# Performance work log

Measured on AMD Instinct MI355X. Metric: run time of the kernel, lower is better.

The kernel has to match this reference:

```python
import jax, jax.numpy as jnp
import numpy as np

B, N, DIM, T, H, DH = 4, 2048, 512, 16, 8, 64
EPS = 1e-5


def setup_inputs() -> dict:
    key = jax.random.key(0)
    ks = jax.random.split(key, 7)
    x = jax.random.normal(ks[0], (B, N, DIM), dtype=jnp.float32)
    # time-distance matrix, e.g. months between scans, in [0, 24)
    R = jax.random.uniform(ks[1], (B, T, T), dtype=jnp.float32) * 24.0
    gamma = jnp.ones((DIM,), dtype=jnp.float32)
    beta = jnp.zeros((DIM,), dtype=jnp.float32)
    W_qkv = jax.random.normal(ks[2], (DIM, 3 * H * DH), dtype=jnp.float32) * 0.02
    W_out = jax.random.normal(ks[3], (H * DH, DIM), dtype=jnp.float32) * 0.02
    a = jax.random.uniform(ks[4], (H,), dtype=jnp.float32)          # torch.rand(heads)
    c = 12.0 * jax.random.uniform(ks[5], (H,), dtype=jnp.float32)   # 12 * torch.rand(heads)
    return {"x": x, "R": R, "gamma": gamma, "beta": beta,
            "W_qkv": W_qkv, "W_out": W_out, "a": a, "c": c}


def reference(x, R, gamma, beta, W_qkv, W_out, a, c):
    b, n, dim = x.shape
    t = R.shape[-1]
    num_patches = n // t
    scale = DH ** -0.5

    # LayerNorm
    mu = jnp.mean(x, axis=-1, keepdims=True)
    var = jnp.mean(jnp.square(x - mu), axis=-1, keepdims=True)
    xn = (x - mu) * jax.lax.rsqrt(var + EPS) * gamma + beta

    # QKV projection -> [b, h, n, d]
    qkv = xn @ W_qkv  # [b, n, 3*h*d]
    q, k, v = jnp.split(qkv, 3, axis=-1)
    def to_heads(z):
        return z.reshape(b, n, H, DH).transpose(0, 2, 1, 3)
    q, k, v = to_heads(q), to_heads(k), to_heads(v)

    # attention scores with ReLU then learned sigmoid time-decay mask
    dots = jnp.einsum('bhnd,bhmd->bhnm', q, k) * scale
    dots = jax.nn.relu(dots)

    # flipped-sigmoid decay: 1 / (1 + exp(|a|*R - |c|)), per head  -> [b, h, t, t]
    decay = 1.0 / (1.0 + jnp.exp(jnp.abs(a)[None, :, None, None] * R[:, None, :, :]
                                 - jnp.abs(c)[None, :, None, None]))
    # expand timepoint mask to token resolution (repeat_interleave on both axes)
    decay = jnp.repeat(jnp.repeat(decay, num_patches, axis=2), num_patches, axis=3)

    attn = jax.nn.softmax(dots * decay, axis=-1)
    out = jnp.einsum('bhnm,bhmd->bhnd', attn, v)
    out = out.transpose(0, 2, 1, 3).reshape(b, n, H * DH)
    return out @ W_out  # dropout is identity at eval
```

## Files before the change

### kernel.cpp

```cpp
#include <hip/hip_runtime.h>
#include <math.h>

#define B_   4
#define N_   2048
#define DIM_ 512
#define T_   16
#define H_   8
#define DH_  64

typedef unsigned short ushort_t;
typedef __attribute__((ext_vector_type(8))) short bf16x8;
typedef __attribute__((ext_vector_type(16))) float f32x16;

__device__ inline ushort_t bf16_rn(float x) {
  unsigned u = __builtin_bit_cast(unsigned, x);
  u += 0x7FFFu + ((u >> 16) & 1u);
  return (ushort_t)(u >> 16);
}
__device__ inline float bf16f(ushort_t h) {
  return __builtin_bit_cast(float, (unsigned)h << 16);
}
__device__ inline unsigned pack2(ushort_t a, ushort_t b) {
  return (unsigned)a | ((unsigned)b << 16);
}
__device__ inline void split2(float x, ushort_t &h, ushort_t &l) {
  h = bf16_rn(x);
  l = bf16_rn(x - bf16f(h));
}
__device__ inline unsigned cvt_pk_bf16(float lo, float hi) {
  unsigned r;
  asm("v_cvt_pk_bf16_f32 %0, %1, %2" : "=v"(r) : "v"(lo), "v"(hi));
  return r;
}
__device__ inline void permlane32_swap(unsigned &x, unsigned &y) {
  asm volatile("v_permlane32_swap_b32 %0, %1" : "+v"(x), "+v"(y));
}
__device__ inline void gload_lds16(const ushort_t* g, ushort_t* l) {
  __builtin_amdgcn_global_load_lds(
      (const __attribute__((address_space(1))) unsigned int*)(g),
      (__attribute__((address_space(3))) unsigned int*)(l),
      16, 0, 0);
}

__global__ __launch_bounds__(256) void prep_kernel(
    const float* __restrict__ x, const float* __restrict__ gamma,
    const float* __restrict__ beta, const float* __restrict__ Wqkv,
    const float* __restrict__ Wout,
    ushort_t* __restrict__ xnh, ushort_t* __restrict__ xnl,
    ushort_t* __restrict__ wqh, ushort_t* __restrict__ wql,
    ushort_t* __restrict__ woh, ushort_t* __restrict__ wol) {
  __shared__ float Ts[64][68];
  int bidx = blockIdx.x;
  int tid = threadIdx.x;
  if (bidx < 256) {
    const float* src; ushort_t* dh; ushort_t* dl; int Nn, n0, k0;
    if (bidx < 192) {
      src = Wqkv; dh = wqh; dl = wql; Nn = 1536;
      n0 = (bidx % 24) * 64; k0 = (bidx / 24) * 64;
    } else {
      int l = bidx - 192;
      src = Wout; dh = woh; dl = wol; Nn = 512;
      n0 = (l % 8) * 64; k0 = (l / 8) * 64;
    }
#pragma unroll
    for (int it = 0; it < 4; ++it) {
      int idx = tid + it * 256;
      int r = idx >> 4, c4 = (idx & 15) * 4;
      *(float4*)&Ts[r][c4] = *(const float4*)&src[(size_t)(k0 + r) * Nn + n0 + c4];
    }
    __syncthreads();
#pragma unroll
    for (int it = 0; it < 2; ++it) {
      int idx = tid + it * 256;
      int n = idx >> 3, kc = (idx & 7) * 8;
      ushort_t hs[8], ls[8];
#pragma unroll
      for (int j = 0; j < 8; ++j) split2(Ts[kc + j][n], hs[j], ls[j]);
      uint4 uh, ul;
      uh.x = pack2(hs[0], hs[1]); uh.y = pack2(hs[2], hs[3]);
      uh.z = pack2(hs[4], hs[5]); uh.w = pack2(hs[6], hs[7]);
      ul.x = pack2(ls[0], ls[1]); ul.y = pack2(ls[2], ls[3]);
      ul.z = pack2(ls[4], ls[5]); ul.w = pack2(ls[6], ls[7]);
      size_t o = (size_t)(n0 + n) * 512 + k0 + kc;
      *(uint4*)&dh[o] = uh;
      *(uint4*)&dl[o] = ul;
    }
  } else {
    int row  = (bidx - 256) * 4 + (tid >> 6);
    int lane = tid & 63;
    const float4* xr = (const float4*)(x + (size_t)row * DIM_);
    float4 v0 = xr[lane * 2 + 0];
    float4 v1 = xr[lane * 2 + 1];
    float s  = v0.x + v0.y + v0.z + v0.w + v1.x + v1.y + v1.z + v1.w;
    float ss = v0.x*v0.x + v0.y*v0.y + v0.z*v0.z + v0.w*v0.w
             + v1.x*v1.x + v1.y*v1.y + v1.z*v1.z + v1.w*v1.w;
#pragma unroll
    for (int off = 32; off > 0; off >>= 1) {
      s  += __shfl_xor(s, off);
      ss += __shfl_xor(ss, off);
    }
    float mu  = s * (1.0f / DIM_);
    float var = ss * (1.0f / DIM_) - mu * mu;
    float rstd = rsqrtf(var + 1e-5f);
    float4 g0 = *(const float4*)&gamma[lane * 8];
    float4 g1 = *(const float4*)&gamma[lane * 8 + 4];
    float4 b0 = *(const float4*)&beta[lane * 8];
    float4 b1 = *(const float4*)&beta[lane * 8 + 4];
    float xv[8] = {v0.x, v0.y, v0.z, v0.w, v1.x, v1.y, v1.z, v1.w};
    float gv[8] = {g0.x, g0.y, g0.z, g0.w, g1.x, g1.y, g1.z, g1.w};
    float bv[8] = {b0.x, b0.y, b0.z, b0.w, b1.x, b1.y, b1.z, b1.w};
    ushort_t hs[8], ls[8];
#pragma unroll
    for (int j = 0; j < 8; ++j) {
      float xn = (xv[j] - mu) * rstd * gv[j] + bv[j];
      split2(xn, hs[j], ls[j]);
    }
    uint4 uh, ul;
    uh.x = pack2(hs[0], hs[1]); uh.y = pack2(hs[2], hs[3]);
    uh.z = pack2(hs[4], hs[5]); uh.w = pack2(hs[6], hs[7]);
    ul.x = pack2(ls[0], ls[1]); ul.y = pack2(ls[2], ls[3]);
    ul.z = pack2(ls[4], ls[5]); ul.w = pack2(ls[6], ls[7]);
    size_t o = (size_t)row * DIM_ + lane * 8;
    *(uint4*)&xnh[o] = uh;
    *(uint4*)&xnl[o] = ul;
  }
}

__global__ __launch_bounds__(256) void qkv_gemm_mfma(
    const ushort_t* __restrict__ xnh, const ushort_t* __restrict__ xnl,
    const ushort_t* __restrict__ wth, const ushort_t* __restrict__ wtl,
    ushort_t* __restrict__ qh, ushort_t* __restrict__ ql,
    ushort_t* __restrict__ kho, ushort_t* __restrict__ klo,
    ushort_t* __restrict__ vt) {
  __shared__ ushort_t Ah[128 * 40], Al[128 * 40], Bh[128 * 40], Bl[128 * 40];
  int tid = threadIdx.x;
  int w = tid >> 6, lane = tid & 63, l31 = lane & 31, g = lane >> 5;
  int wm = w >> 1, wn = w & 1;
  int idx = blockIdx.x;
  int xcd = idx & 7, local = idx >> 3;
  int n0 = (local % 12) * 128;
  int m0 = ((local / 12) * 8 + xcd) * 128;

  f32x16 acc[2][2];
#pragma unroll
  for (int i = 0; i < 2; ++i)
#pragma unroll
    for (int j = 0; j < 2; ++j)
#pragma unroll
      for (int e = 0; e < 16; ++e) acc[i][j][e] = 0.0f;

  int fm[2], fc[2];
#pragma unroll
  for (int it = 0; it < 2; ++it) {
    int f = tid + it * 256;
    fm[it] = f >> 2;
    fc[it] = (f & 3) * 8;
  }

#pragma unroll 1
  for (int kt = 0; kt < 16; ++kt) {
    __syncthreads();
#pragma unroll
    for (int it = 0; it < 2; ++it) {
      size_t ao = (size_t)(m0 + fm[it]) * 512 + kt * 32 + fc[it];
      size_t bo = (size_t)(n0 + fm[it]) * 512 + kt * 32 + fc[it];
      uint4 tah = *(const uint4*)&xnh[ao];
      uint4 tal = *(const uint4*)&xnl[ao];
      uint4 tbh = *(const uint4*)&wth[bo];
      uint4 tbl = *(const uint4*)&wtl[bo];
      int o = fm[it] * 40 + fc[it];
      *(uint4*)&Ah[o] = tah;
      *(uint4*)&Al[o] = tal;
      *(uint4*)&Bh[o] = tbh;
      *(uint4*)&Bl[o] = tbl;
    }
    __syncthreads();
#pragma unroll
    for (int kc = 0; kc < 2; ++kc) {
      int off = kc * 16 + 8 * g;
      bf16x8 afh[2], afl[2], bfh[2], bfl[2];
#pragma unroll
      for (int rb = 0; rb < 2; ++rb) {
        int r = (wm * 64 + rb * 32 + l31) * 40 + off;
        afh[rb] = *(const bf16x8*)&Ah[r];
        afl[rb] = *(const bf16x8*)&Al[r];
      }
#pragma unroll
      for (int cb = 0; cb < 2; ++cb) {
        int r = (wn * 64 + cb * 32 + l31) * 40 + off;
        bfh[cb] = *(const bf16x8*)&Bh[r];
        bfl[cb] = *(const bf16x8*)&Bl[r];
      }
#pragma unroll
      for (int rb = 0; rb < 2; ++rb)
#pragma unroll
        for (int cb = 0; cb < 2; ++cb) {
          acc[rb][cb] = __builtin_amdgcn_mfma_f32_32x32x16_bf16(afh[rb], bfh[cb], acc[rb][cb], 0, 0, 0);
          acc[rb][cb] = __builtin_amdgcn_mfma_f32_32x32x16_bf16(afh[rb], bfl[cb], acc[rb][cb], 0, 0, 0);
          acc[rb][cb] = __builtin_amdgcn_mfma_f32_32x32x16_bf16(afl[rb], bfh[cb], acc[rb][cb], 0, 0, 0);
        }
    }
  }

  int part = n0 >> 9;
#pragma unroll
  for (int rb = 0; rb < 2; ++rb) {
    int m_base = m0 + wm * 64 + rb * 32;
#pragma unroll
    for (int cb = 0; cb < 2; ++cb) {
      int n_g = n0 + wn * 64 + cb * 32 + l31;
      int rem = n_g & 511, hh = rem >> 6, d = rem & 63;
      if (part == 2) {
#pragma unroll
        for (int grp = 0; grp < 4; ++grp) {
          int m_g = m_base + grp * 8 + 4 * g;
          int bb = m_g >> 11, tok = m_g & 2047;
          uint2 pk;
          pk.x = pack2(bf16_rn(acc[rb][cb][grp * 4 + 0]), bf16_rn(acc[rb][cb][grp * 4 + 1]));
          pk.y = pack2(bf16_rn(acc[rb][cb][grp * 4 + 2]), bf16_rn(acc[rb][cb][grp * 4 + 3]));
          *(uint2*)&vt[((size_t)(bb * 8 + hh) * 64 + d) * 2048 + tok] = pk;
        }
      } else {
        float sc = (part == 0) ? 0.125f : 1.0f;
        ushort_t* dsth = (part == 0) ? qh : kho;
        ushort_t* dstl = (part == 0) ? ql : klo;
#pragma unroll
        for (int reg = 0; reg < 16; ++reg) {
          int row = (reg & 3) + 8 * (reg >> 2) + 4 * g;
          int m_g = m_base + row;
          int bb = m_g >> 11, tok = m_g & 2047;
          ushort_t hi, lo;
          split2(acc[rb][cb][reg] * sc, hi, lo);
          size_t addr = ((size_t)(bb * 8 + hh) * 2048 + tok) * 64 + d;
          dsth[addr] = hi;
          dstl[addr] = lo;
        }
      }
    }
  }
}

__global__ __launch_bounds__(256) void attn_mfma(
    const ushort_t* __restrict__ qh, const ushort_t* __restrict__ ql,
    const ushort_t* __restrict__ kho, const ushort_t* __restrict__ klo,
    const ushort_t* __restrict__ vt, const float* __restrict__ R,
    const float* __restrict__ a, const float* __restrict__ c,
    ushort_t* __restrict__ aoh, ushort_t* __restrict__ aol) {
  __shared__ __align__(16) ushort_t KhS[2 * 4608];
  __shared__ __align__(16) ushort_t KlS[2 * 4608];
  __shared__ __align__(16) ushort_t VtS[2 * 4608];
  __shared__ float rsS[128];
  __shared__ float decl2S[16];

  int tid = threadIdx.x;
  int w = tid >> 6, lane = tid & 63, l31 = lane & 31, g = lane >> 5;
  int bh = blockIdx.x;
  int qt = blockIdx.y;
  int b = bh >> 3, h = bh & 7;

  int qrow = qt * 128 + w * 32 + l31;
  size_t qoff = ((size_t)bh * 2048 + qrow) * 64;
  bf16x8 qfh[4], qfl[4];
#pragma unroll
  for (int d0i = 0; d0i < 4; ++d0i) {
    qfh[d0i] = *(const bf16x8*)&qh[qoff + d0i * 16 + 8 * g];
    qfl[d0i] = *(const bf16x8*)&ql[qoff + d0i * 16 + 8 * g];
  }

  const ushort_t* kbase = kho + (size_t)bh * 2048 * 64;
  const ushort_t* lbase = klo + (size_t)bh * 2048 * 64;
  const ushort_t* vbase = vt + (size_t)bh * 64 * 2048;

  if (tid < 16) {
    float aab = fabsf(a[h]);
    float cab = fabsf(c[h]);
    float Rv = R[b * (T_ * T_) + qt * T_ + tid];
    decl2S[tid] = 1.4426950408889634f / (1.0f + __expf(aab * Rv - cab));
  }

  int r_[3], j8_[3];
#pragma unroll
  for (int i = 0; i < 3; ++i) {
    int ch = (i < 2) ? (w + i * 4) : 8;
    int u = ch * 512 + lane * 8;
    int r = u / 72;
    int j = (u - r * 72) >> 3;
    r_[i] = r;
    j8_[i] = (j == 8) ? 0 : (j << 3);
  }
  int a8 = (w < 3) ? w : 0;

  f32x16 oacc[2];
#pragma unroll
  for (int t = 0; t < 2; ++t)
#pragma unroll
    for (int i = 0; i < 16; ++i) oacc[t][i] = 0.0f;
  float rsp[4] = {0.0f, 0.0f, 0.0f, 0.0f};

  {
#pragma unroll
    for (int i = 0; i < 2; ++i) {
      int cb = (w + i * 4) * 512;
      gload_lds16(&kbase[(size_t)r_[i] * 64 + j8_[i]], &KhS[cb]);
      gload_lds16(&lbase[(size_t)r_[i] * 64 + j8_[i]], &KlS[cb]);
      gload_lds16(&vbase[(size_t)r_[i] * 2048 + j8_[i]], &VtS[cb]);
    }
    int cb8 = 8 * 512;
    if (a8 == 0)      gload_lds16(&kbase[(size_t)r_[2] * 64 + j8_[2]], &KhS[cb8]);
    else if (a8 == 1) gload_lds16(&lbase[(size_t)r_[2] * 64 + j8_[2]], &KlS[cb8]);
    else              gload_lds16(&vbase[(size_t)r_[2] * 2048 + j8_[2]], &VtS[cb8]);
  }
  __syncthreads();

  int cur = 0;

#pragma unroll 1
  for (int kt = 0; kt < 32; ++kt) {
    if (kt + 1 < 32) {
      int lb = (cur ^ 1) * 4608;
      int kk = kt + 1;
#pragma unroll
      for (int i = 0; i < 2; ++i) {
        int cb = lb + (w + i * 4) * 512;
        gload_lds16(&kbase[(size_t)kk * 4096 + r_[i] * 64 + j8_[i]], &KhS[cb]);
        gload_lds16(&lbase[(size_t)kk * 4096 + r_[i] * 64 + j8_[i]], &KlS[cb]);
        gload_lds16(&vbase[(size_t)r_[i] * 2048 + kk * 64 + j8_[i]], &VtS[cb]);
      }
      int cb8 = lb + 8 * 512;
      if (a8 == 0)      gload_lds16(&kbase[(size_t)kk * 4096 + r_[2] * 64 + j8_[2]], &KhS[cb8]);
      else if (a8 == 1) gload_lds16(&lbase[(size_t)kk * 4096 + r_[2] * 64 + j8_[2]], &KlS[cb8]);
      else              gload_lds16(&vbase[(size_t)r_[2] * 2048 + kk * 64 + j8_[2]], &VtS[cb8]);
      asm volatile("s_waitcnt vmcnt(7)" ::: "memory");
    } else {
      asm volatile("s_waitcnt vmcnt(0)" ::: "memory");
    }
    __builtin_amdgcn_s_barrier();

    float decl2 = decl2S[kt >> 1];
    int kb = cur * 4608;

    bf16x8 pa[4];
#pragma unroll
    for (int khalf = 0; khalf < 2; ++khalf) {
      f32x16 sacc;
#pragma unroll
      for (int i = 0; i < 16; ++i) sacc[i] = 0.0f;
      int krow = kb + (khalf * 32 + l31) * 72;
#pragma unroll
      for (int d0i = 0; d0i < 4; ++d0i) {
        int off = krow + d0i * 16 + 8 * g;
        bf16x8 kfh = *(const bf16x8*)&KhS[off];
        bf16x8 kfl = *(const bf16x8*)&KlS[off];
        sacc = __builtin_amdgcn_mfma_f32_32x32x16_bf16(kfh, qfh[d0i], sacc, 0, 0, 0);
        sacc = __builtin_amdgcn_mfma_f32_32x32x16_bf16(kfl, qfh[d0i], sacc, 0, 0, 0);
        sacc = __builtin_amdgcn_mfma_f32_32x32x16_bf16(kfh, qfl[d0i], sacc, 0, 0, 0);
      }
#pragma unroll
      for (int reg = 0; reg < 16; ++reg) {
        float pvv = exp2f(fmaxf(sacc[reg], 0.0f) * decl2);
        rsp[reg & 3] += pvv;
        sacc[reg] = pvv;
      }
#pragma unroll
      for (int hf = 0; hf < 2; ++hf) {
        unsigned d0 = cvt_pk_bf16(sacc[hf * 8 + 0], sacc[hf * 8 + 1]);
        unsigned d1 = cvt_pk_bf16(sacc[hf * 8 + 2], sacc[hf * 8 + 3]);
        unsigned d2 = cvt_pk_bf16(sacc[hf * 8 + 4], sacc[hf * 8 + 5]);
        unsigned d3 = cvt_pk_bf16(sacc[hf * 8 + 6], sacc[hf * 8 + 7]);
        permlane32_swap(d0, d2);
        permlane32_swap(d1, d3);
        uint4 u; u.x = d0; u.y = d1; u.z = d2; u.w = d3;
        pa[khalf * 2 + hf] = __builtin_bit_cast(bf16x8, u);
      }
    }

#pragma unroll
    for (int dt = 0; dt < 2; ++dt) {
      int vrow = kb + (dt * 32 + l31) * 72;
#pragma unroll
      for (int kc = 0; kc < 4; ++kc) {
        bf16x8 vf = *(const bf16x8*)&VtS[vrow + kc * 16 + 8 * g];
        oacc[dt] = __builtin_amdgcn_mfma_f32_32x32x16_bf16(pa[kc], vf, oacc[dt], 0, 0, 0);
      }
    }

    __builtin_amdgcn_s_barrier();
    cur ^= 1;
  }

  float rs = (rsp[0] + rsp[1]) + (rsp[2] + rsp[3]);
  rs += __shfl_xor(rs, 32);
  rsS[w * 32 + l31] = rs;

#pragma unroll
  for (int reg = 0; reg < 16; ++reg) {
    int row = (reg & 3) + 8 * (reg >> 2) + 4 * g;
    float invs = 1.0f / rsS[w * 32 + row];
    int tok = qt * 128 + w * 32 + row;
#pragma unroll
    for (int dt = 0; dt < 2; ++dt) {
      int d = dt * 32 + l31;
      ushort_t hi, lo;
      split2(oacc[dt][reg] * invs, hi, lo);
      size_t addr = ((size_t)b * 2048 + tok) * 512 + h * 64 + d;
      aoh[addr] = hi;
      aol[addr] = lo;
    }
  }
}

__global__ __launch_bounds__(256) void out_gemm_mfma(
    const ushort_t* __restrict__ ah, const ushort_t* __restrict__ al,
    const ushort_t* __restrict__ wth, const ushort_t* __restrict__ wtl,
    float* __restrict__ out) {
  __shared__ ushort_t Ah[128 * 40], Al[128 * 40], Bh[128 * 40], Bl[128 * 40];
  int tid = threadIdx.x;
  int w = tid >> 6, lane = tid & 63, l31 = lane & 31, g = lane >> 5;
  int wm = w >> 1, wn = w & 1;
  int idx = blockIdx.x;
  int xcd = idx & 7, local = idx >> 3;
  int n0 = (local & 3) * 128;
  int m0 = ((local >> 2) * 8 + xcd) * 128;

  f32x16 acc[2][2];
#pragma unroll
  for (int i = 0; i < 2; ++i)
#pragma unroll
    for (int j = 0; j < 2; ++j)
#pragma unroll
      for (int e = 0; e < 16; ++e) acc[i][j][e] = 0.0f;

  int fm[2], fc[2];
#pragma unroll
  for (int it = 0; it < 2; ++it) {
    int f = tid + it * 256;
    fm[it] = f >> 2;
    fc[it] = (f & 3) * 8;
  }

#pragma unroll 1
  for (int kt = 0; kt < 16; ++kt) {
    __syncthreads();
#pragma unroll
    for (int it = 0; it < 2; ++it) {
      size_t ao = (size_t)(m0 + fm[it]) * 512 + kt * 32 + fc[it];
      size_t bo = (size_t)(n0 + fm[it]) * 512 + kt * 32 + fc[it];
      uint4 tah = *(const uint4*)&ah[ao];
      uint4 tal = *(const uint4*)&al[ao];
      uint4 tbh = *(const uint4*)&wth[bo];
      uint4 tbl = *(const uint4*)&wtl[bo];
      int o = fm[it] * 40 + fc[it];
      *(uint4*)&Ah[o] = tah;
      *(uint4*)&Al[o] = tal;
      *(uint4*)&Bh[o] = tbh;
      *(uint4*)&Bl[o] = tbl;
    }
    __syncthreads();
#pragma unroll
    for (int kc = 0; kc < 2; ++kc) {
      int off = kc * 16 + 8 * g;
      bf16x8 afh[2], afl[2], bfh[2], bfl[2];
#pragma unroll
      for (int rb = 0; rb < 2; ++rb) {
        int r = (wm * 64 + rb * 32 + l31) * 40 + off;
        afh[rb] = *(const bf16x8*)&Ah[r];
        afl[rb] = *(const bf16x8*)&Al[r];
      }
#pragma unroll
      for (int cb = 0; cb < 2; ++cb) {
        int r = (wn * 64 + cb * 32 + l31) * 40 + off;
        bfh[cb] = *(const bf16x8*)&Bh[r];
        bfl[cb] = *(const bf16x8*)&Bl[r];
      }
#pragma unroll
      for (int rb = 0; rb < 2; ++rb)
#pragma unroll
        for (int cb = 0; cb < 2; ++cb) {
          acc[rb][cb] = __builtin_amdgcn_mfma_f32_32x32x16_bf16(afh[rb], bfh[cb], acc[rb][cb], 0, 0, 0);
          acc[rb][cb] = __builtin_amdgcn_mfma_f32_32x32x16_bf16(afh[rb], bfl[cb], acc[rb][cb], 0, 0, 0);
          acc[rb][cb] = __builtin_amdgcn_mfma_f32_32x32x16_bf16(afl[rb], bfh[cb], acc[rb][cb], 0, 0, 0);
        }
    }
  }

#pragma unroll
  for (int rb = 0; rb < 2; ++rb) {
    int m_base = m0 + wm * 64 + rb * 32;
#pragma unroll
    for (int cb = 0; cb < 2; ++cb) {
      int n_g = n0 + wn * 64 + cb * 32 + l31;
#pragma unroll
      for (int reg = 0; reg < 16; ++reg) {
        int row = (reg & 3) + 8 * (reg >> 2) + 4 * g;
        out[(size_t)(m_base + row) * 512 + n_g] = acc[rb][cb][reg];
      }
    }
  }
}

extern "C" void kernel_launch(void* const* d_in, const int* in_sizes, int n_in,
                              void* d_out, int out_size, void* d_ws, size_t ws_size,
                              hipStream_t stream) {
  (void)in_sizes; (void)n_in;
  const float* x     = (const float*)d_in[0];
  const float* R     = (const float*)d_in[1];
  const float* gamma = (const float*)d_in[2];
  const float* beta  = (const float*)d_in[3];
  const float* Wqkv  = (const float*)d_in[4];
  const float* Wout  = (const float*)d_in[5];
  const float* av    = (const float*)d_in[6];
  const float* cv    = (const float*)d_in[7];
  float* out = (float*)d_out;

  const size_t EL  = (size_t)B_ * N_ * DIM_;
  const size_t SZT = EL * sizeof(ushort_t);

  char* p = (char*)d_ws;
  ushort_t* wqh = (ushort_t*)p;                  p += (size_t)1536 * 512 * 2;
  ushort_t* wql = (ushort_t*)p;                  p += (size_t)1536 * 512 * 2;
  ushort_t* woh = (ushort_t*)p;                  p += (size_t)512 * 512 * 2;
  ushort_t* wol = (ushort_t*)p;                  p += (size_t)512 * 512 * 2;
  ushort_t* qhb = (ushort_t*)p;                  p += SZT;
  ushort_t* qlb = (ushort_t*)p;                  p += SZT;
  ushort_t* khb = (ushort_t*)p;                  p += SZT;
  ushort_t* klb = (ushort_t*)p;                  p += SZT;
  ushort_t* vtb = (ushort_t*)p;                  p += SZT;
  size_t base_need = (size_t)(p - (char*)d_ws);
  size_t needA = base_need + 2 * SZT;

  bool planA = (ws_size >= needA);
  ushort_t* xnh = planA ? (ushort_t*)p : (ushort_t*)d_out;
  ushort_t* xnl = xnh + EL;
  float* gemm_dst = planA ? out : (float*)qhb;

  prep_kernel<<<dim3(2304), dim3(256), 0, stream>>>(x, gamma, beta, Wqkv, Wout,
                                                    xnh, xnl, wqh, wql, woh, wol);
  qkv_gemm_mfma<<<dim3(768), dim3(256), 0, stream>>>(xnh, xnl, wqh, wql,
                                                     qhb, qlb, khb, klb, vtb);
  attn_mfma<<<dim3(32, 16), dim3(256), 0, stream>>>(qhb, qlb, khb, klb, vtb,
                                                    R, av, cv, xnh, xnl);
  out_gemm_mfma<<<dim3(256), dim3(256), 0, stream>>>(xnh, xnl, woh, wol, gemm_dst);
  if (!planA) {
    hipMemcpyAsync(out, gemm_dst, (size_t)out_size * sizeof(float),
                   hipMemcpyDeviceToDevice, stream);
  }
}
```

Measured before the change: 250.2 us.

## Preload K/V LDS fragments to registers before issuing next-tile prefetch in attention loop

Each key-tile iteration of the attention kernel now starts by reading all K-high, K-low and V^T fragments for the current buffer from LDS into registers. Only then does it issue the async global-to-LDS prefetch for the next tile. The explicit vmcnt wait and the barrier at the top of the loop are removed, and the MFMAs consume the register copies, so LDS reads and MFMA work are meant to overlap with the prefetch. The kernel also gains a two-blocks-per-CU launch bound. Holding about 24 vector fragments live raises register pressure and may cause spills under the tighter bound. Dropping the vmcnt wait risks reading an LDS buffer before its async load has landed, unless the compiler inserts the wait itself.

```diff
diff --git a/kernel.cpp b/kernel.cpp
--- a/kernel.cpp
+++ b/kernel.cpp
@@ -240,7 +240,7 @@
   }
 }
 
-__global__ __launch_bounds__(256) void attn_mfma(
+__global__ __launch_bounds__(256, 2) void attn_mfma(
     const ushort_t* __restrict__ qh, const ushort_t* __restrict__ ql,
     const ushort_t* __restrict__ kho, const ushort_t* __restrict__ klo,
     const ushort_t* __restrict__ vt, const float* __restrict__ R,
@@ -316,6 +316,29 @@
 
 #pragma unroll 1
   for (int kt = 0; kt < 32; ++kt) {
+    int kb = cur * 4608;
+
+    float decl2 = decl2S[kt >> 1];
+    bf16x8 kfh[2][4], kfl[2][4], vf[2][4];
+#pragma unroll
+    for (int khalf = 0; khalf < 2; ++khalf) {
+      int krow = kb + (khalf * 32 + l31) * 72;
+#pragma unroll
+      for (int d0i = 0; d0i < 4; ++d0i) {
+        int off = krow + d0i * 16 + 8 * g;
+        kfh[khalf][d0i] = *(const bf16x8*)&KhS[off];
+        kfl[khalf][d0i] = *(const bf16x8*)&KlS[off];
+      }
+    }
+#pragma unroll
+    for (int dt = 0; dt < 2; ++dt) {
+      int vrow = kb + (dt * 32 + l31) * 72;
+#pragma unroll
+      for (int kc = 0; kc < 4; ++kc)
+        vf[dt][kc] = *(const bf16x8*)&VtS[vrow + kc * 16 + 8 * g];
+    }
+    __builtin_amdgcn_sched_barrier(0);
+
     if (kt + 1 < 32) {
       int lb = (cur ^ 1) * 4608;
       int kk = kt + 1;
@@ -330,14 +353,8 @@
       if (a8 == 0)      gload_lds16(&kbase[(size_t)kk * 4096 + r_[2] * 64 + j8_[2]], &KhS[cb8]);
       else if (a8 == 1) gload_lds16(&lbase[(size_t)kk * 4096 + r_[2] * 64 + j8_[2]], &KlS[cb8]);
       else              gload_lds16(&vbase[(size_t)r_[2] * 2048 + kk * 64 + j8_[2]], &VtS[cb8]);
-      asm volatile("s_waitcnt vmcnt(7)" ::: "memory");
-    } else {
-      asm volatile("s_waitcnt vmcnt(0)" ::: "memory");
-    }
-    __builtin_amdgcn_s_barrier();
-
-    float decl2 = decl2S[kt >> 1];
-    int kb = cur * 4608;
+    }
+    __builtin_amdgcn_sched_barrier(0);
 
     bf16x8 pa[4];
 #pragma unroll
@@ -345,15 +362,11 @@
       f32x16 sacc;
 #pragma unroll
       for (int i = 0; i < 16; ++i) sacc[i] = 0.0f;
-      int krow = kb + (khalf * 32 + l31) * 72;
 #pragma unroll
       for (int d0i = 0; d0i < 4; ++d0i) {
-        int off = krow + d0i * 16 + 8 * g;
-        bf16x8 kfh = *(const bf16x8*)&KhS[off];
-        bf16x8 kfl = *(const bf16x8*)&KlS[off];
-        sacc = __builtin_amdgcn_mfma_f32_32x32x16_bf16(kfh, qfh[d0i], sacc, 0, 0, 0);
-        sacc = __builtin_amdgcn_mfma_f32_32x32x16_bf16(kfl, qfh[d0i], sacc, 0, 0, 0);
-        sacc = __builtin_amdgcn_mfma_f32_32x32x16_bf16(kfh, qfl[d0i], sacc, 0, 0, 0);
+        sacc = __builtin_amdgcn_mfma_f32_32x32x16_bf16(kfh[khalf][d0i], qfh[d0i], sacc, 0, 0, 0);
+        sacc = __builtin_amdgcn_mfma_f32_32x32x16_bf16(kfl[khalf][d0i], qfh[d0i], sacc, 0, 0, 0);
+        sacc = __builtin_amdgcn_mfma_f32_32x32x16_bf16(kfh[khalf][d0i], qfl[d0i], sacc, 0, 0, 0);
       }
 #pragma unroll
       for (int reg = 0; reg < 16; ++reg) {
@@ -375,14 +388,10 @@
     }
 
 #pragma unroll
-    for (int dt = 0; dt < 2; ++dt) {
-      int vrow = kb + (dt * 32 + l31) * 72;
-#pragma unroll
-      for (int kc = 0; kc < 4; ++kc) {
-        bf16x8 vf = *(const bf16x8*)&VtS[vrow + kc * 16 + 8 * g];
-        oacc[dt] = __builtin_amdgcn_mfma_f32_32x32x16_bf16(pa[kc], vf, oacc[dt], 0, 0, 0);
-      }
-    }
+    for (int dt = 0; dt < 2; ++dt)
+#pragma unroll
+      for (int kc = 0; kc < 4; ++kc)
+        oacc[dt] = __builtin_amdgcn_mfma_f32_32x32x16_bf16(pa[kc], vf[dt][kc], oacc[dt], 0, 0, 0);
 
     __builtin_amdgcn_s_barrier();
     cur ^= 1;
```

Result: faster. 235.6 us (-5.8%).
